# Performance work log

Measured on AMD Instinct MI355X. Metric: run time of the kernel, lower is better.

## Reference

```python
import jax, jax.numpy as jnp
import numpy as np

N_NODES = 50000
N_EDGES = 800000
H_DIM = 128
N_REL = 40
N_BASES = 4


def setup_inputs() -> dict:
    key = jax.random.key(0)
    ks = jax.random.split(key, 9)
    h = jax.random.normal(ks[0], (N_NODES, H_DIM), jnp.float32)
    norm = jax.random.uniform(ks[1], (N_EDGES, 1), jnp.float32)
    basis_w = jax.random.normal(ks[2], (N_BASES, H_DIM, H_DIM), jnp.float32) * 0.05
    w_comp = jax.random.normal(ks[3], (N_REL, N_BASES), jnp.float32) * 0.5
    loop_w = jax.random.normal(ks[4], (H_DIM, H_DIM), jnp.float32) * 0.05
    bias = jax.random.normal(ks[5], (H_DIM,), jnp.float32) * 0.05
    src = jax.random.randint(ks[6], (N_EDGES,), 0, N_NODES, jnp.int32)
    dst = jax.random.randint(ks[7], (N_EDGES,), 0, N_NODES, jnp.int32)
    etype = jax.random.randint(ks[8], (N_EDGES,), 0, N_REL, jnp.int32)
    return {"h": h, "norm": norm, "basis_w": basis_w, "w_comp": w_comp,
            "loop_w": loop_w, "bias": bias, "src": src, "dst": dst, "etype": etype}


def reference(h, norm, basis_w, w_comp, loop_w, bias, src, dst, etype):
    # RelGraphConv with 'basis' regularizer, one layer (num_hidden_layers=1):
    #   W_r = sum_b w_comp[r, b] * basis_w[b]
    #   m_e = (h[src_e] @ W_{etype_e}) * norm_e
    #   agg[v] = sum_{e: dst_e = v} m_e
    #   out = relu(agg + bias + h @ loop_w)   (dropout = 0)
    # Contraction reordered for memory efficiency: scatter-add per-basis
    # scaled source features first (node-level), then apply small basis GEMMs.
    n = h.shape[0]
    n_bases = basis_w.shape[0]
    coeff = w_comp[etype] * norm          # [E, B] per-edge basis coefficients * norm
    h_src = h[src]                        # [E, D] edge-gathered source features
    agg = jnp.zeros((n, basis_w.shape[2]), dtype=h.dtype)
    for b in range(n_bases):              # small fixed loop over bases
        s_b = jax.ops.segment_sum(coeff[:, b:b + 1] * h_src, dst, num_segments=n)  # [N, D]
        agg = agg + s_b @ basis_w[b]
    return jax.nn.relu(agg + bias + h @ loop_w)
```

## Files before the change

### kernel.cpp

```cpp
#include <hip/hip_runtime.h>
#include <stdint.h>

#define N_NODES 50000
#define N_EDGES 800000
#define H_DIM 128
#define N_REL 40
#define N_BASES 4
#define N_RANGES 196
#define EP_BLOCKS 200
#define EDGES_PER_BLK 4000
#define STAGE_CAP 5120

typedef __attribute__((ext_vector_type(8))) short bf16x8;
typedef __attribute__((ext_vector_type(4))) float f32x4;

__device__ __forceinline__ unsigned short f2bf(float f) {
    unsigned int u = __float_as_uint(f);
    unsigned int r = u + 0x7fffu + ((u >> 16) & 1u);
    return (unsigned short)(r >> 16);
}

__global__ __launch_bounds__(256) void prep_kernel(
        const float* __restrict__ h,
        const float* __restrict__ basis_w, const float* __restrict__ loop_w,
        const int* __restrict__ src, const int* __restrict__ dst,
        const int* __restrict__ etype, const float* __restrict__ norm,
        unsigned short* __restrict__ A, unsigned short* __restrict__ wt3,
        uint2* __restrict__ pkd, int* __restrict__ gcnt,
        unsigned* __restrict__ sorted_src, float4* __restrict__ sorted_cf) {
    int bid = blockIdx.x;
    if (bid < 3125) {
        int t = bid * 256 + threadIdx.x;
        int row = t >> 4;
        int cb = (t & 15) * 8;
        const float* p = h + (size_t)row * 128 + cb;
        float4 a0 = ((const float4*)p)[0];
        float4 a1 = ((const float4*)p)[1];
        bf16x8 o;
        o[0] = (short)f2bf(a0.x); o[1] = (short)f2bf(a0.y);
        o[2] = (short)f2bf(a0.z); o[3] = (short)f2bf(a0.w);
        o[4] = (short)f2bf(a1.x); o[5] = (short)f2bf(a1.y);
        o[6] = (short)f2bf(a1.z); o[7] = (short)f2bf(a1.w);
        *(bf16x8*)(A + (size_t)row * H_DIM + cb) = o;
    } else if (bid < 3130) {
        int mat = bid - 3125;
        const float* srcm = (mat < 4) ? (basis_w + mat * 16384) : loop_w;
        int koff = (mat < 4) ? (128 + mat * 128) : 0;
        int t = threadIdx.x;
#pragma unroll
        for (int i = 0; i < 16; ++i) {
            int f = t + i * 256;
            int k = f >> 5;
            int j4 = (f & 31) * 4;
            float4 v = ((const float4*)srcm)[f];
            int kg = koff + k;
            int ks = kg >> 5;
            int quad = (kg >> 3) & 3;
            int jj = kg & 7;
            float vv[4] = {v.x, v.y, v.z, v.w};
#pragma unroll
            for (int d = 0; d < 4; ++d) {
                int j = j4 + d;
                int cg = j >> 4;
                int n16 = j & 15;
                wt3[(size_t)((ks * 8 + cg) * 64 + quad * 16 + n16) * 8 + jj] =
                    f2bf(vv[d]);
            }
        }
    } else {
        __shared__ int lhist[N_RANGES];
        int blk = bid - 3130;
        int t = threadIdx.x;
        if (t < N_RANGES) lhist[t] = 0;
        if (blk == 0 && t >= 240) {
            int k = t - 240;
            sorted_src[N_EDGES + k] = 0u;
            sorted_cf[N_EDGES + k] = make_float4(0.f, 0.f, 0.f, 0.f);
        }
        __syncthreads();
        int e0 = blk * EDGES_PER_BLK;
        for (int i = t; i < EDGES_PER_BLK; i += 256) {
            int e = e0 + i;
            int d = dst[e];
            unsigned int nbf = f2bf(norm[e]);
            pkd[e] = make_uint2((unsigned)src[e] | ((unsigned)etype[e] << 20),
                                (unsigned)d | (nbf << 17));
            atomicAdd(&lhist[d >> 8], 1);
        }
        __syncthreads();
        if (t < N_RANGES) gcnt[blk * N_RANGES + t] = lhist[t];
    }
}

__global__ __launch_bounds__(512) void binscatter(
        const uint2* __restrict__ pkd, const int* __restrict__ gcnt,
        uint2* __restrict__ bucketed) {
    __shared__ int lcur[N_RANGES];
    __shared__ int wsum[8];
    int t = threadIdx.x, lane = t & 63, w = t >> 6;
    int b = blockIdx.x;
    int tot = 0, pre = 0;
    if (t < N_RANGES) {
        for (int bb = 0; bb < EP_BLOCKS; ++bb) {
            int g = gcnt[bb * N_RANGES + t];
            tot += g;
            if (bb < b) pre += g;
        }
    }
    int x = (t < N_RANGES) ? tot : 0;
    int v = x;
#pragma unroll
    for (int d = 1; d < 64; d <<= 1) {
        int y = __shfl_up(v, d);
        if (lane >= d) v += y;
    }
    if (lane == 63) wsum[w] = v;
    __syncthreads();
    int wpre = 0;
#pragma unroll
    for (int ww = 0; ww < 7; ++ww)
        if (w > ww) wpre += wsum[ww];
    if (t < N_RANGES)
        lcur[t] = (wpre + v - x) + pre;
    __syncthreads();
    int e0 = b * EDGES_PER_BLK;
    for (int i = t; i < EDGES_PER_BLK; i += 512) {
        uint2 p = pkd[e0 + i];
        int r = (p.y & 0x1FFFF) >> 8;
        int pos = atomicAdd(&lcur[r], 1);
        bucketed[pos] = p;
    }
}

__global__ __launch_bounds__(512) void bucket_sort(
        const int* __restrict__ gcnt, const uint2* __restrict__ bucketed,
        const float* __restrict__ w_comp,
        unsigned* __restrict__ sorted_src, float4* __restrict__ sorted_cf,
        int* __restrict__ offs) {
    __shared__ int hist[256];
    __shared__ int cur[256];
    __shared__ int wsum[8];
    __shared__ int sbeg;
    __shared__ int stot;
    __shared__ uint2 stage[STAGE_CAP];
    int r = blockIdx.x;
    int t = threadIdx.x, lane = t & 63, w = t >> 6;
    int tot = 0;
    if (t < N_RANGES)
        for (int bb = 0; bb < EP_BLOCKS; ++bb)
            tot += gcnt[bb * N_RANGES + t];
    int x = (t < N_RANGES) ? tot : 0;
    int v = x;
#pragma unroll
    for (int d = 1; d < 64; d <<= 1) {
        int y = __shfl_up(v, d);
        if (lane >= d) v += y;
    }
    if (lane == 63) wsum[w] = v;
    if (t < 256) hist[t] = 0;
    __syncthreads();
    int wpre = 0;
#pragma unroll
    for (int ww = 0; ww < 7; ++ww)
        if (w > ww) wpre += wsum[ww];
    if (t == r) { sbeg = wpre + v - x; stot = x; }
    __syncthreads();
    int begin = sbeg;
    int end = begin + stot;
    int n = end - begin;
    for (int i = begin + t; i < end; i += 512)
        atomicAdd(&hist[bucketed[i].y & 255], 1);
    __syncthreads();
    int x2 = (t < 256) ? hist[t] : 0;
    int v2 = x2;
#pragma unroll
    for (int d = 1; d < 64; d <<= 1) {
        int y = __shfl_up(v2, d);
        if (lane >= d) v2 += y;
    }
    if (lane == 63) wsum[w] = v2;
    __syncthreads();
    int wpre2 = 0;
#pragma unroll
    for (int ww = 0; ww < 3; ++ww)
        if (w > ww) wpre2 += wsum[ww];
    if (t < 256) {
        int excl_rel = wpre2 + v2 - x2;
        int node = r * 256 + t;
        if (node < N_NODES) offs[node] = begin + excl_rel;
        cur[t] = excl_rel;
    }
    if (r == N_RANGES - 1 && t == 0) offs[N_NODES] = N_EDGES;
    __syncthreads();
    if (n <= STAGE_CAP) {
        for (int i = begin + t; i < end; i += 512) {
            uint2 p = bucketed[i];
            int pos = atomicAdd(&cur[p.y & 255], 1);
            stage[pos] = make_uint2(p.x, (p.y >> 17) << 16);
        }
        __syncthreads();
        for (int i = t; i < n; i += 512) {
            uint2 p = stage[i];
            float nm = __uint_as_float(p.y);
            float4 wc = ((const float4*)w_comp)[p.x >> 20];
            sorted_src[begin + i] = p.x & 0xFFFFF;
            sorted_cf[begin + i] =
                make_float4(wc.x * nm, wc.y * nm, wc.z * nm, wc.w * nm);
        }
    } else {
        for (int i = begin + t; i < end; i += 512) {
            uint2 p = bucketed[i];
            int pos = atomicAdd(&cur[p.y & 255], 1);
            float nm = __uint_as_float((p.y >> 17) << 16);
            float4 wc = ((const float4*)w_comp)[p.x >> 20];
            sorted_src[begin + pos] = p.x & 0xFFFFF;
            sorted_cf[begin + pos] =
                make_float4(wc.x * nm, wc.y * nm, wc.z * nm, wc.w * nm);
        }
    }
}

__global__ __launch_bounds__(512, 8) void agg_gemm(
        const int* __restrict__ offs, const unsigned* __restrict__ ssrc,
        const float4* __restrict__ scf,
        const unsigned short* __restrict__ Ab,
        const unsigned short* __restrict__ wt3,
        const float* __restrict__ bias, float* __restrict__ out) {
    __shared__ __align__(16) unsigned short S[32 * 640];
    int wv = threadIdx.x >> 6;
    int lane = threadIdx.x & 63;
    int nbase = blockIdx.x * 32;
    const unsigned int* Au = (const unsigned int*)Ab;

#pragma unroll
    for (int q = 0; q < 4; ++q) {
        int row = (wv << 2) + q;
        int v = __builtin_amdgcn_readfirstlane(nbase + row);
        float a0l = 0.f, a0h = 0.f, a1l = 0.f, a1h = 0.f;
        float a2l = 0.f, a2h = 0.f, a3l = 0.f, a3h = 0.f;
        unsigned int hb = 0u;
        if (v < N_NODES) {
            hb = Au[(size_t)v * 64 + lane];
            int begin = __builtin_amdgcn_readfirstlane(offs[v]);
            int end   = __builtin_amdgcn_readfirstlane(offs[v + 1]);
            for (int j = begin; j < end; j += 8) {
                int rem = end - j;
                unsigned su[8];
                float4 c[8];
#pragma unroll
                for (int k = 0; k < 8; ++k) su[k] = ssrc[j + k];
#pragma unroll
                for (int k = 0; k < 8; ++k) c[k] = scf[j + k];
                if (rem < 8) {
#pragma unroll
                    for (int k = 0; k < 8; ++k)
                        if (k >= rem) {
                            su[k] = 0u;
                            c[k] = make_float4(0.f, 0.f, 0.f, 0.f);
                        }
                }
                unsigned u[8];
#pragma unroll
                for (int k = 0; k < 8; ++k)
                    u[k] = Au[(size_t)su[k] * 64 + lane];
#pragma unroll
                for (int k = 0; k < 8; ++k) {
                    float lo = __uint_as_float(u[k] << 16);
                    float hi = __uint_as_float(u[k] & 0xffff0000u);
                    a0l += c[k].x * lo; a0h += c[k].x * hi;
                    a1l += c[k].y * lo; a1h += c[k].y * hi;
                    a2l += c[k].z * lo; a2h += c[k].z * hi;
                    a3l += c[k].w * lo; a3h += c[k].w * hi;
                }
            }
        }
        char* rp = (char*)S + row * 1280;
        int swz = (row & 7) << 4;
        *(unsigned int*)(rp + ((lane * 4) ^ swz)) = hb;
        *(unsigned int*)(rp + ((256 + lane * 4) ^ swz)) =
            (unsigned int)f2bf(a0l) | ((unsigned int)f2bf(a0h) << 16);
        *(unsigned int*)(rp + ((512 + lane * 4) ^ swz)) =
            (unsigned int)f2bf(a1l) | ((unsigned int)f2bf(a1h) << 16);
        *(unsigned int*)(rp + ((768 + lane * 4) ^ swz)) =
            (unsigned int)f2bf(a2l) | ((unsigned int)f2bf(a2h) << 16);
        *(unsigned int*)(rp + ((1024 + lane * 4) ^ swz)) =
            (unsigned int)f2bf(a3l) | ((unsigned int)f2bf(a3h) << 16);
    }
    __syncthreads();

    int n16 = lane & 15;
    int quad = lane >> 4;
    f32x4 acc0 = (f32x4)0.f, acc1 = (f32x4)0.f;

    const char* s0p = (const char*)S + n16 * 1280;
    const char* s1p = s0p + 16 * 1280;
    int swz2 = (n16 & 7) << 4;
    const unsigned short* bwp = wt3 + (size_t)wv * 512 + (size_t)lane * 8;

#pragma unroll
    for (int ks = 0; ks < 20; ++ks) {
        int off = (ks * 64 + quad * 16) ^ swz2;
        bf16x8 a0 = *(const bf16x8*)(s0p + off);
        bf16x8 a1 = *(const bf16x8*)(s1p + off);
        bf16x8 b  = *(const bf16x8*)(bwp + (size_t)ks * 4096);
        acc0 = __builtin_amdgcn_mfma_f32_16x16x32_bf16(a0, b, acc0, 0, 0, 0);
        acc1 = __builtin_amdgcn_mfma_f32_16x16x32_bf16(a1, b, acc1, 0, 0, 0);
    }

    int col = (wv << 4) + n16;
    float bv = bias[col];
#pragma unroll
    for (int rg = 0; rg < 4; ++rg) {
        int r0 = nbase + quad * 4 + rg;
        if (r0 < N_NODES)
            out[(size_t)r0 * H_DIM + col] = fmaxf(acc0[rg] + bv, 0.f);
        int r1 = nbase + 16 + quad * 4 + rg;
        if (r1 < N_NODES)
            out[(size_t)r1 * H_DIM + col] = fmaxf(acc1[rg] + bv, 0.f);
    }
}

extern "C" void kernel_launch(void* const* d_in, const int* in_sizes, int n_in,
                              void* d_out, int out_size, void* d_ws, size_t ws_size,
                              hipStream_t stream) {
    const float* h       = (const float*)d_in[0];
    const float* norm    = (const float*)d_in[1];
    const float* basis_w = (const float*)d_in[2];
    const float* w_comp  = (const float*)d_in[3];
    const float* loop_w  = (const float*)d_in[4];
    const float* bias    = (const float*)d_in[5];
    const int*   src     = (const int*)d_in[6];
    const int*   dst     = (const int*)d_in[7];
    const int*   etype   = (const int*)d_in[8];
    float* out = (float*)d_out;

    char* base = (char*)d_ws;
    unsigned short* wt3       = (unsigned short*)(base + 0);
    unsigned short* A         = (unsigned short*)(base + 163840);
    int*            offs      = (int*)(base + 12963840);
    uint2*          pkd       = (uint2*)(base + 13163848);
    uint2*          bucketed  = (uint2*)(base + 19563848);
    float4*         sorted_cf = (float4*)(base + 25963856);
    unsigned*       sorted_src= (unsigned*)(base + 38764112);
    int*            gcnt      = (int*)(base + 41964176);

    prep_kernel<<<3330, 256, 0, stream>>>(h, basis_w, loop_w,
                                          src, dst, etype, norm,
                                          A, wt3, pkd, gcnt,
                                          sorted_src, sorted_cf);
    binscatter<<<EP_BLOCKS, 512, 0, stream>>>(pkd, gcnt, bucketed);
    bucket_sort<<<N_RANGES, 512, 0, stream>>>(gcnt, bucketed, w_comp,
                                              sorted_src, sorted_cf, offs);
    agg_gemm<<<1563, 512, 0, stream>>>(offs, sorted_src, sorted_cf,
                                       A, wt3, bias, out);
}
```

Measured before the change: 180.1 us.

## Replace two-level bucket sort with global degree-count CSR and software-pipeline gathers

Drops the two-pass bucketed counting sort and builds CSR directly: global atomic degree counts, a per-range scan that recomputes its prefix base from the degree array, and a direct atomic scatter of edges into place. This removes the bucketed staging buffer and one full pass over edges. In exchange it relies on heavily contended global atomics, and edge order within each node becomes nondeterministic. The aggregation loop is also double-buffered so the next 8-edge gather is issued before the current batch is accumulated, to hide gather latency.

New measurement: 261.9 us. +45.4%, slower.

```diff
diff --git a/kernel.cpp b/kernel.cpp
--- a/kernel.cpp
+++ b/kernel.cpp
@@ -7,9 +7,7 @@
 #define N_REL 40
 #define N_BASES 4
 #define N_RANGES 196
-#define EP_BLOCKS 200
 #define EDGES_PER_BLK 4000
-#define STAGE_CAP 5120
 
 typedef __attribute__((ext_vector_type(8))) short bf16x8;
 typedef __attribute__((ext_vector_type(4))) float f32x4;
@@ -18,6 +16,11 @@
     unsigned int u = __float_as_uint(f);
     unsigned int r = u + 0x7fffu + ((u >> 16) & 1u);
     return (unsigned short)(r >> 16);
+}
+
+__global__ __launch_bounds__(512) void zero_deg(int* __restrict__ deg) {
+    int i = blockIdx.x * 512 + threadIdx.x;
+    if (i < N_NODES) deg[i] = 0;
 }
 
 __global__ __launch_bounds__(256) void prep_kernel(
@@ -26,7 +29,7 @@
         const int* __restrict__ src, const int* __restrict__ dst,
         const int* __restrict__ etype, const float* __restrict__ norm,
         unsigned short* __restrict__ A, unsigned short* __restrict__ wt3,
-        uint2* __restrict__ pkd, int* __restrict__ gcnt,
+        uint2* __restrict__ pkd, int* __restrict__ deg,
         unsigned* __restrict__ sorted_src, float4* __restrict__ sorted_cf) {
     int bid = blockIdx.x;
     if (bid < 3125) {
@@ -68,16 +71,13 @@
             }
         }
     } else {
-        __shared__ int lhist[N_RANGES];
         int blk = bid - 3130;
         int t = threadIdx.x;
-        if (t < N_RANGES) lhist[t] = 0;
         if (blk == 0 && t >= 240) {
             int k = t - 240;
             sorted_src[N_EDGES + k] = 0u;
             sorted_cf[N_EDGES + k] = make_float4(0.f, 0.f, 0.f, 0.f);
         }
-        __syncthreads();
         int e0 = blk * EDGES_PER_BLK;
         for (int i = t; i < EDGES_PER_BLK; i += 256) {
             int e = e0 + i;
@@ -85,139 +85,66 @@
             unsigned int nbf = f2bf(norm[e]);
             pkd[e] = make_uint2((unsigned)src[e] | ((unsigned)etype[e] << 20),
                                 (unsigned)d | (nbf << 17));
-            atomicAdd(&lhist[d >> 8], 1);
-        }
-        __syncthreads();
-        if (t < N_RANGES) gcnt[blk * N_RANGES + t] = lhist[t];
-    }
-}
-
-__global__ __launch_bounds__(512) void binscatter(
-        const uint2* __restrict__ pkd, const int* __restrict__ gcnt,
-        uint2* __restrict__ bucketed) {
-    __shared__ int lcur[N_RANGES];
-    __shared__ int wsum[8];
+            atomicAdd(&deg[d], 1);
+        }
+    }
+}
+
+__global__ __launch_bounds__(512) void scan_offs(
+        const int* __restrict__ deg, int* __restrict__ offs,
+        int* __restrict__ cur) {
+    __shared__ int red[8];
+    __shared__ int wsum[4];
+    int r = blockIdx.x;
     int t = threadIdx.x, lane = t & 63, w = t >> 6;
-    int b = blockIdx.x;
-    int tot = 0, pre = 0;
-    if (t < N_RANGES) {
-        for (int bb = 0; bb < EP_BLOCKS; ++bb) {
-            int g = gcnt[bb * N_RANGES + t];
-            tot += g;
-            if (bb < b) pre += g;
-        }
-    }
-    int x = (t < N_RANGES) ? tot : 0;
+    int lim = r * 256;
+    int s = 0;
+    for (int i = t; i < lim; i += 512) s += deg[i];
+#pragma unroll
+    for (int d = 32; d; d >>= 1) s += __shfl_down(s, d);
+    if (lane == 0) red[w] = s;
+    __syncthreads();
+    int base = 0;
+#pragma unroll
+    for (int ww = 0; ww < 8; ++ww) base += red[ww];
+    int node = r * 256 + t;
+    int x = 0;
+    if (t < 256) x = (node < N_NODES) ? deg[node] : 0;
     int v = x;
 #pragma unroll
     for (int d = 1; d < 64; d <<= 1) {
         int y = __shfl_up(v, d);
         if (lane >= d) v += y;
     }
-    if (lane == 63) wsum[w] = v;
+    if (t < 256 && lane == 63) wsum[w] = v;
     __syncthreads();
-    int wpre = 0;
-#pragma unroll
-    for (int ww = 0; ww < 7; ++ww)
-        if (w > ww) wpre += wsum[ww];
-    if (t < N_RANGES)
-        lcur[t] = (wpre + v - x) + pre;
-    __syncthreads();
-    int e0 = b * EDGES_PER_BLK;
-    for (int i = t; i < EDGES_PER_BLK; i += 512) {
-        uint2 p = pkd[e0 + i];
-        int r = (p.y & 0x1FFFF) >> 8;
-        int pos = atomicAdd(&lcur[r], 1);
-        bucketed[pos] = p;
-    }
-}
-
-__global__ __launch_bounds__(512) void bucket_sort(
-        const int* __restrict__ gcnt, const uint2* __restrict__ bucketed,
-        const float* __restrict__ w_comp,
-        unsigned* __restrict__ sorted_src, float4* __restrict__ sorted_cf,
-        int* __restrict__ offs) {
-    __shared__ int hist[256];
-    __shared__ int cur[256];
-    __shared__ int wsum[8];
-    __shared__ int sbeg;
-    __shared__ int stot;
-    __shared__ uint2 stage[STAGE_CAP];
-    int r = blockIdx.x;
-    int t = threadIdx.x, lane = t & 63, w = t >> 6;
-    int tot = 0;
-    if (t < N_RANGES)
-        for (int bb = 0; bb < EP_BLOCKS; ++bb)
-            tot += gcnt[bb * N_RANGES + t];
-    int x = (t < N_RANGES) ? tot : 0;
-    int v = x;
-#pragma unroll
-    for (int d = 1; d < 64; d <<= 1) {
-        int y = __shfl_up(v, d);
-        if (lane >= d) v += y;
-    }
-    if (lane == 63) wsum[w] = v;
-    if (t < 256) hist[t] = 0;
-    __syncthreads();
-    int wpre = 0;
-#pragma unroll
-    for (int ww = 0; ww < 7; ++ww)
-        if (w > ww) wpre += wsum[ww];
-    if (t == r) { sbeg = wpre + v - x; stot = x; }
-    __syncthreads();
-    int begin = sbeg;
-    int end = begin + stot;
-    int n = end - begin;
-    for (int i = begin + t; i < end; i += 512)
-        atomicAdd(&hist[bucketed[i].y & 255], 1);
-    __syncthreads();
-    int x2 = (t < 256) ? hist[t] : 0;
-    int v2 = x2;
-#pragma unroll
-    for (int d = 1; d < 64; d <<= 1) {
-        int y = __shfl_up(v2, d);
-        if (lane >= d) v2 += y;
-    }
-    if (lane == 63) wsum[w] = v2;
-    __syncthreads();
-    int wpre2 = 0;
-#pragma unroll
-    for (int ww = 0; ww < 3; ++ww)
-        if (w > ww) wpre2 += wsum[ww];
     if (t < 256) {
-        int excl_rel = wpre2 + v2 - x2;
-        int node = r * 256 + t;
-        if (node < N_NODES) offs[node] = begin + excl_rel;
-        cur[t] = excl_rel;
+        int wpre = 0;
+        if (w > 0) wpre += wsum[0];
+        if (w > 1) wpre += wsum[1];
+        if (w > 2) wpre += wsum[2];
+        int excl = base + wpre + v - x;
+        if (node < N_NODES) {
+            offs[node] = excl;
+            cur[node] = excl;
+        }
     }
     if (r == N_RANGES - 1 && t == 0) offs[N_NODES] = N_EDGES;
-    __syncthreads();
-    if (n <= STAGE_CAP) {
-        for (int i = begin + t; i < end; i += 512) {
-            uint2 p = bucketed[i];
-            int pos = atomicAdd(&cur[p.y & 255], 1);
-            stage[pos] = make_uint2(p.x, (p.y >> 17) << 16);
-        }
-        __syncthreads();
-        for (int i = t; i < n; i += 512) {
-            uint2 p = stage[i];
-            float nm = __uint_as_float(p.y);
-            float4 wc = ((const float4*)w_comp)[p.x >> 20];
-            sorted_src[begin + i] = p.x & 0xFFFFF;
-            sorted_cf[begin + i] =
-                make_float4(wc.x * nm, wc.y * nm, wc.z * nm, wc.w * nm);
-        }
-    } else {
-        for (int i = begin + t; i < end; i += 512) {
-            uint2 p = bucketed[i];
-            int pos = atomicAdd(&cur[p.y & 255], 1);
-            float nm = __uint_as_float((p.y >> 17) << 16);
-            float4 wc = ((const float4*)w_comp)[p.x >> 20];
-            sorted_src[begin + pos] = p.x & 0xFFFFF;
-            sorted_cf[begin + pos] =
-                make_float4(wc.x * nm, wc.y * nm, wc.z * nm, wc.w * nm);
-        }
-    }
+}
+
+__global__ __launch_bounds__(256) void scatter_kernel(
+        const uint2* __restrict__ pkd, const float* __restrict__ w_comp,
+        int* __restrict__ cur, unsigned* __restrict__ sorted_src,
+        float4* __restrict__ sorted_cf) {
+    int e = blockIdx.x * 256 + threadIdx.x;
+    if (e >= N_EDGES) return;
+    uint2 p = pkd[e];
+    int d = p.y & 0x1FFFF;
+    float nm = __uint_as_float((p.y >> 17) << 16);
+    float4 wc = ((const float4*)w_comp)[p.x >> 20];
+    int pos = atomicAdd(&cur[d], 1);
+    sorted_src[pos] = p.x & 0xFFFFF;
+    sorted_cf[pos] = make_float4(wc.x * nm, wc.y * nm, wc.z * nm, wc.w * nm);
 }
 
 __global__ __launch_bounds__(512, 8) void agg_gemm(
@@ -232,6 +159,27 @@
     int nbase = blockIdx.x * 32;
     const unsigned int* Au = (const unsigned int*)Ab;
 
+#define CONSUME(U, JJ) do {                                                  \
+        float4 c[8];                                                         \
+        int rem = end - (JJ);                                                \
+        _Pragma("unroll")                                                    \
+        for (int k = 0; k < 8; ++k) c[k] = scf[(JJ) + k];                    \
+        if (rem < 8) {                                                       \
+            _Pragma("unroll")                                                \
+            for (int k = 0; k < 8; ++k)                                      \
+                if (k >= rem) c[k] = make_float4(0.f, 0.f, 0.f, 0.f);        \
+        }                                                                    \
+        _Pragma("unroll")                                                    \
+        for (int k = 0; k < 8; ++k) {                                        \
+            float lo = __uint_as_float(U[k] << 16);                          \
+            float hi = __uint_as_float(U[k] & 0xffff0000u);                  \
+            a0l += c[k].x * lo; a0h += c[k].x * hi;                          \
+            a1l += c[k].y * lo; a1h += c[k].y * hi;                          \
+            a2l += c[k].z * lo; a2h += c[k].z * hi;                          \
+            a3l += c[k].w * lo; a3h += c[k].w * hi;                          \
+        }                                                                    \
+    } while (0)
+
 #pragma unroll
     for (int q = 0; q < 4; ++q) {
         int row = (wv << 2) + q;
@@ -243,35 +191,37 @@
             hb = Au[(size_t)v * 64 + lane];
             int begin = __builtin_amdgcn_readfirstlane(offs[v]);
             int end   = __builtin_amdgcn_readfirstlane(offs[v + 1]);
-            for (int j = begin; j < end; j += 8) {
-                int rem = end - j;
-                unsigned su[8];
-                float4 c[8];
-#pragma unroll
-                for (int k = 0; k < 8; ++k) su[k] = ssrc[j + k];
-#pragma unroll
-                for (int k = 0; k < 8; ++k) c[k] = scf[j + k];
-                if (rem < 8) {
-#pragma unroll
-                    for (int k = 0; k < 8; ++k)
-                        if (k >= rem) {
-                            su[k] = 0u;
-                            c[k] = make_float4(0.f, 0.f, 0.f, 0.f);
-                        }
+            if (begin < end) {
+                unsigned suA[8], suB[8], uA[8], uB[8];
+                int jA = begin, jB = 0;
+#pragma unroll
+                for (int k = 0; k < 8; ++k) suA[k] = ssrc[jA + k];
+#pragma unroll
+                for (int k = 0; k < 8; ++k)
+                    uA[k] = Au[(size_t)suA[k] * 64 + lane];
+                int curA = 1;
+                for (int jn = begin + 8; jn < end; jn += 8) {
+                    if (curA) {
+                        jB = jn;
+#pragma unroll
+                        for (int k = 0; k < 8; ++k) suB[k] = ssrc[jB + k];
+#pragma unroll
+                        for (int k = 0; k < 8; ++k)
+                            uB[k] = Au[(size_t)suB[k] * 64 + lane];
+                        CONSUME(uA, jA);
+                    } else {
+                        jA = jn;
+#pragma unroll
+                        for (int k = 0; k < 8; ++k) suA[k] = ssrc[jA + k];
+#pragma unroll
+                        for (int k = 0; k < 8; ++k)
+                            uA[k] = Au[(size_t)suA[k] * 64 + lane];
+                        CONSUME(uB, jB);
+                    }
+                    curA ^= 1;
                 }
-                unsigned u[8];
-#pragma unroll
-                for (int k = 0; k < 8; ++k)
-                    u[k] = Au[(size_t)su[k] * 64 + lane];
-#pragma unroll
-                for (int k = 0; k < 8; ++k) {
-                    float lo = __uint_as_float(u[k] << 16);
-                    float hi = __uint_as_float(u[k] & 0xffff0000u);
-                    a0l += c[k].x * lo; a0h += c[k].x * hi;
-                    a1l += c[k].y * lo; a1h += c[k].y * hi;
-                    a2l += c[k].z * lo; a2h += c[k].z * hi;
-                    a3l += c[k].w * lo; a3h += c[k].w * hi;
-                }
+                if (curA) CONSUME(uA, jA);
+                else      CONSUME(uB, jB);
             }
         }
         char* rp = (char*)S + row * 1280;
@@ -286,6 +236,7 @@
         *(unsigned int*)(rp + ((1024 + lane * 4) ^ swz)) =
             (unsigned int)f2bf(a3l) | ((unsigned int)f2bf(a3h) << 16);
     }
+#undef CONSUME
     __syncthreads();
 
     int n16 = lane & 15;
@@ -339,18 +290,19 @@
     unsigned short* A         = (unsigned short*)(base + 163840);
     int*            offs      = (int*)(base + 12963840);
     uint2*          pkd       = (uint2*)(base + 13163848);
-    uint2*          bucketed  = (uint2*)(base + 19563848);
-    float4*         sorted_cf = (float4*)(base + 25963856);
-    unsigned*       sorted_src= (unsigned*)(base + 38764112);
-    int*            gcnt      = (int*)(base + 41964176);
-
+    float4*         sorted_cf = (float4*)(base + 19563856);
+    unsigned*       sorted_src= (unsigned*)(base + 32364112);
+    int*            deg       = (int*)(base + 35564176);
+    int*            cur       = (int*)(base + 35764176);
+
+    zero_deg<<<98, 512, 0, stream>>>(deg);
     prep_kernel<<<3330, 256, 0, stream>>>(h, basis_w, loop_w,
                                           src, dst, etype, norm,
-                                          A, wt3, pkd, gcnt,
+                                          A, wt3, pkd, deg,
                                           sorted_src, sorted_cf);
-    binscatter<<<EP_BLOCKS, 512, 0, stream>>>(pkd, gcnt, bucketed);
-    bucket_sort<<<N_RANGES, 512, 0, stream>>>(gcnt, bucketed, w_comp,
-                                              sorted_src, sorted_cf, offs);
+    scan_offs<<<N_RANGES, 512, 0, stream>>>(deg, offs, cur);
+    scatter_kernel<<<3125, 256, 0, stream>>>(pkd, w_comp, cur,
+                                             sorted_src, sorted_cf);
     agg_gemm<<<1563, 512, 0, stream>>>(offs, sorted_src, sorted_cf,
                                        A, wt3, bias, out);
 }
```

## Move h cast and weight repack into binscatter launch, shrink edge blocks

Applied to the files above, without the earlier changes.

The edge packing and histogram now run in their own small kernel. The fp32-to-bf16 cast of h and the weight repacking move into the same launch as the bin-scatter, so the bandwidth-heavy cast overlaps with the scatter. Edges per block are halved and the block count doubled for more parallelism in pack and scatter. The cost is that every scatter block now scans a gcnt prefix array twice as long (400 entries per range).

Result: no change. 179.2 us (-0.5%).

```diff
diff --git a/kernel.cpp b/kernel.cpp
--- a/kernel.cpp
+++ b/kernel.cpp
@@ -7,9 +7,10 @@
 #define N_REL 40
 #define N_BASES 4
 #define N_RANGES 196
-#define EP_BLOCKS 200
-#define EDGES_PER_BLK 4000
+#define EP_BLOCKS 400
+#define EDGES_PER_BLK 2000
 #define STAGE_CAP 5120
+#define CAST_BLOCKS 1563
 
 typedef __attribute__((ext_vector_type(8))) short bf16x8;
 typedef __attribute__((ext_vector_type(4))) float f32x4;
@@ -20,36 +21,100 @@
     return (unsigned short)(r >> 16);
 }
 
-__global__ __launch_bounds__(256) void prep_kernel(
+__global__ __launch_bounds__(512) void edge_pack(
+        const int* __restrict__ src, const int* __restrict__ dst,
+        const int* __restrict__ etype, const float* __restrict__ norm,
+        uint2* __restrict__ pkd, int* __restrict__ gcnt,
+        unsigned* __restrict__ sorted_src, float4* __restrict__ sorted_cf) {
+    __shared__ int lhist[N_RANGES];
+    int blk = blockIdx.x;
+    int t = threadIdx.x;
+    if (t < N_RANGES) lhist[t] = 0;
+    if (blk == 0 && t >= 496) {
+        int k = t - 496;
+        sorted_src[N_EDGES + k] = 0u;
+        sorted_cf[N_EDGES + k] = make_float4(0.f, 0.f, 0.f, 0.f);
+    }
+    __syncthreads();
+    int e0 = blk * EDGES_PER_BLK;
+    for (int i = t; i < EDGES_PER_BLK; i += 512) {
+        int e = e0 + i;
+        int d = dst[e];
+        unsigned int nbf = f2bf(norm[e]);
+        pkd[e] = make_uint2((unsigned)src[e] | ((unsigned)etype[e] << 20),
+                            (unsigned)d | (nbf << 17));
+        atomicAdd(&lhist[d >> 8], 1);
+    }
+    __syncthreads();
+    if (t < N_RANGES) gcnt[blk * N_RANGES + t] = lhist[t];
+}
+
+__global__ __launch_bounds__(512) void stage2(
         const float* __restrict__ h,
         const float* __restrict__ basis_w, const float* __restrict__ loop_w,
-        const int* __restrict__ src, const int* __restrict__ dst,
-        const int* __restrict__ etype, const float* __restrict__ norm,
+        const uint2* __restrict__ pkd, const int* __restrict__ gcnt,
         unsigned short* __restrict__ A, unsigned short* __restrict__ wt3,
-        uint2* __restrict__ pkd, int* __restrict__ gcnt,
-        unsigned* __restrict__ sorted_src, float4* __restrict__ sorted_cf) {
+        uint2* __restrict__ bucketed) {
+    __shared__ int lcur[N_RANGES];
+    __shared__ int wsum[8];
     int bid = blockIdx.x;
-    if (bid < 3125) {
-        int t = bid * 256 + threadIdx.x;
-        int row = t >> 4;
-        int cb = (t & 15) * 8;
-        const float* p = h + (size_t)row * 128 + cb;
-        float4 a0 = ((const float4*)p)[0];
-        float4 a1 = ((const float4*)p)[1];
-        bf16x8 o;
-        o[0] = (short)f2bf(a0.x); o[1] = (short)f2bf(a0.y);
-        o[2] = (short)f2bf(a0.z); o[3] = (short)f2bf(a0.w);
-        o[4] = (short)f2bf(a1.x); o[5] = (short)f2bf(a1.y);
-        o[6] = (short)f2bf(a1.z); o[7] = (short)f2bf(a1.w);
-        *(bf16x8*)(A + (size_t)row * H_DIM + cb) = o;
-    } else if (bid < 3130) {
-        int mat = bid - 3125;
+    int t = threadIdx.x;
+    if (bid < EP_BLOCKS) {
+        int lane = t & 63, w = t >> 6;
+        int b = bid;
+        int tot = 0, pre = 0;
+        if (t < N_RANGES) {
+            for (int bb = 0; bb < EP_BLOCKS; ++bb) {
+                int g = gcnt[bb * N_RANGES + t];
+                tot += g;
+                if (bb < b) pre += g;
+            }
+        }
+        int x = (t < N_RANGES) ? tot : 0;
+        int v = x;
+#pragma unroll
+        for (int d = 1; d < 64; d <<= 1) {
+            int y = __shfl_up(v, d);
+            if (lane >= d) v += y;
+        }
+        if (lane == 63) wsum[w] = v;
+        __syncthreads();
+        int wpre = 0;
+#pragma unroll
+        for (int ww = 0; ww < 7; ++ww)
+            if (w > ww) wpre += wsum[ww];
+        if (t < N_RANGES)
+            lcur[t] = (wpre + v - x) + pre;
+        __syncthreads();
+        int e0 = b * EDGES_PER_BLK;
+        for (int i = t; i < EDGES_PER_BLK; i += 512) {
+            uint2 p = pkd[e0 + i];
+            int r = (p.y & 0x1FFFF) >> 8;
+            int pos = atomicAdd(&lcur[r], 1);
+            bucketed[pos] = p;
+        }
+    } else if (bid < EP_BLOCKS + CAST_BLOCKS) {
+        int g = (bid - EP_BLOCKS) * 512 + t;
+        if (g < 800000) {
+            int row = g >> 4;
+            int cb = (g & 15) * 8;
+            const float* p = h + (size_t)row * 128 + cb;
+            float4 a0 = ((const float4*)p)[0];
+            float4 a1 = ((const float4*)p)[1];
+            bf16x8 o;
+            o[0] = (short)f2bf(a0.x); o[1] = (short)f2bf(a0.y);
+            o[2] = (short)f2bf(a0.z); o[3] = (short)f2bf(a0.w);
+            o[4] = (short)f2bf(a1.x); o[5] = (short)f2bf(a1.y);
+            o[6] = (short)f2bf(a1.z); o[7] = (short)f2bf(a1.w);
+            *(bf16x8*)(A + (size_t)row * H_DIM + cb) = o;
+        }
+    } else {
+        int mat = bid - EP_BLOCKS - CAST_BLOCKS;
         const float* srcm = (mat < 4) ? (basis_w + mat * 16384) : loop_w;
         int koff = (mat < 4) ? (128 + mat * 128) : 0;
-        int t = threadIdx.x;
-#pragma unroll
-        for (int i = 0; i < 16; ++i) {
-            int f = t + i * 256;
+#pragma unroll
+        for (int i = 0; i < 8; ++i) {
+            int f = t + i * 512;
             int k = f >> 5;
             int j4 = (f & 31) * 4;
             float4 v = ((const float4*)srcm)[f];
@@ -67,68 +132,6 @@
                     f2bf(vv[d]);
             }
         }
-    } else {
-        __shared__ int lhist[N_RANGES];
-        int blk = bid - 3130;
-        int t = threadIdx.x;
-        if (t < N_RANGES) lhist[t] = 0;
-        if (blk == 0 && t >= 240) {
-            int k = t - 240;
-            sorted_src[N_EDGES + k] = 0u;
-            sorted_cf[N_EDGES + k] = make_float4(0.f, 0.f, 0.f, 0.f);
-        }
-        __syncthreads();
-        int e0 = blk * EDGES_PER_BLK;
-        for (int i = t; i < EDGES_PER_BLK; i += 256) {
-            int e = e0 + i;
-            int d = dst[e];
-            unsigned int nbf = f2bf(norm[e]);
-            pkd[e] = make_uint2((unsigned)src[e] | ((unsigned)etype[e] << 20),
-                                (unsigned)d | (nbf << 17));
-            atomicAdd(&lhist[d >> 8], 1);
-        }
-        __syncthreads();
-        if (t < N_RANGES) gcnt[blk * N_RANGES + t] = lhist[t];
-    }
-}
-
-__global__ __launch_bounds__(512) void binscatter(
-        const uint2* __restrict__ pkd, const int* __restrict__ gcnt,
-        uint2* __restrict__ bucketed) {
-    __shared__ int lcur[N_RANGES];
-    __shared__ int wsum[8];
-    int t = threadIdx.x, lane = t & 63, w = t >> 6;
-    int b = blockIdx.x;
-    int tot = 0, pre = 0;
-    if (t < N_RANGES) {
-        for (int bb = 0; bb < EP_BLOCKS; ++bb) {
-            int g = gcnt[bb * N_RANGES + t];
-            tot += g;
-            if (bb < b) pre += g;
-        }
-    }
-    int x = (t < N_RANGES) ? tot : 0;
-    int v = x;
-#pragma unroll
-    for (int d = 1; d < 64; d <<= 1) {
-        int y = __shfl_up(v, d);
-        if (lane >= d) v += y;
-    }
-    if (lane == 63) wsum[w] = v;
-    __syncthreads();
-    int wpre = 0;
-#pragma unroll
-    for (int ww = 0; ww < 7; ++ww)
-        if (w > ww) wpre += wsum[ww];
-    if (t < N_RANGES)
-        lcur[t] = (wpre + v - x) + pre;
-    __syncthreads();
-    int e0 = b * EDGES_PER_BLK;
-    for (int i = t; i < EDGES_PER_BLK; i += 512) {
-        uint2 p = pkd[e0 + i];
-        int r = (p.y & 0x1FFFF) >> 8;
-        int pos = atomicAdd(&lcur[r], 1);
-        bucketed[pos] = p;
     }
 }
 
@@ -344,11 +347,11 @@
     unsigned*       sorted_src= (unsigned*)(base + 38764112);
     int*            gcnt      = (int*)(base + 41964176);
 
-    prep_kernel<<<3330, 256, 0, stream>>>(h, basis_w, loop_w,
-                                          src, dst, etype, norm,
-                                          A, wt3, pkd, gcnt,
-                                          sorted_src, sorted_cf);
-    binscatter<<<EP_BLOCKS, 512, 0, stream>>>(pkd, gcnt, bucketed);
+    edge_pack<<<EP_BLOCKS, 512, 0, stream>>>(src, dst, etype, norm,
+                                             pkd, gcnt,
+                                             sorted_src, sorted_cf);
+    stage2<<<EP_BLOCKS + CAST_BLOCKS + 5, 512, 0, stream>>>(
+        h, basis_w, loop_w, pkd, gcnt, A, wt3, bucketed);
     bucket_sort<<<N_RANGES, 512, 0, stream>>>(gcnt, bucketed, w_comp,
                                               sorted_src, sorted_cf, offs);
     agg_gemm<<<1563, 512, 0, stream>>>(offs, sorted_src, sorted_cf,
```
